# Performance work log

Measured on AMD Instinct MI355X. Metric: run time of the kernel, lower is better.

The kernel has to match this reference:

```python
import jax, jax.numpy as jnp
import numpy as np

CHANNELS = 512
NUM_HEADS = 8
GROUPS = 32
EPS = 1e-5


def setup_inputs() -> dict:
    key = jax.random.key(0)
    ks = jax.random.split(key, 7)
    C = CHANNELS
    x = jax.random.normal(ks[0], (8, C, 32, 32), dtype=jnp.float32)
    gn_weight = jnp.ones((C,), dtype=jnp.float32)
    gn_bias = jnp.zeros((C,), dtype=jnp.float32)
    # Conv1d(C, 3C, k=1) weights ~ N(0, 0.02) per init_weights
    qkv_w = 0.02 * jax.random.normal(ks[1], (3 * C, C), dtype=jnp.float32)
    qkv_b = 0.01 * jax.random.normal(ks[2], (3 * C,), dtype=jnp.float32)
    out_w = 0.02 * jax.random.normal(ks[3], (C, C), dtype=jnp.float32)
    out_b = 0.01 * jax.random.normal(ks[4], (C,), dtype=jnp.float32)
    return {"x": x, "gn_weight": gn_weight, "gn_bias": gn_bias,
            "qkv_w": qkv_w, "qkv_b": qkv_b, "out_w": out_w, "out_b": out_b}


def _forward(x, gn_weight, gn_bias, qkv_w, qkv_b, out_w, out_b):
    n, c, h, w = x.shape
    hw = h * w
    heads = NUM_HEADS
    cph = c // heads
    xs = x.reshape(n, c, hw)  # [N, C, HW]
    # GroupNorm over (channels-in-group, spatial)
    xg = xs.reshape(n, GROUPS, c // GROUPS, hw)
    mean = jnp.mean(xg, axis=(2, 3), keepdims=True)
    var = jnp.var(xg, axis=(2, 3), keepdims=True)
    xn = ((xg - mean) * jax.lax.rsqrt(var + EPS)).reshape(n, c, hw)
    xn = xn * gn_weight[None, :, None] + gn_bias[None, :, None]
    # 1x1 Conv1d QKV projection
    qkv = jnp.einsum('oc,ncl->nol', qkv_w, xn) + qkv_b[None, :, None]  # [N, 3C, HW]
    q, k, v = jnp.split(qkv, 3, axis=1)  # each [N, C, HW]
    q = q.reshape(n * heads, cph, hw)
    k = k.reshape(n * heads, cph, hw)
    v = v.reshape(n * heads, cph, hw)
    scale = 1.0 / np.sqrt(cph).astype(np.float32)
    scores = jnp.einsum('bci,bcj->bij', q, k) * scale  # [NH, HW, HW]
    attn = jax.nn.softmax(scores, axis=-1)
    weighted = jnp.einsum('bij,bcj->bic', attn, v)  # [NH, HW, cph]
    # Faithful to torch: reshape(n, -1, h, w) on [n*heads, hw, cph] layout
    weighted = weighted.reshape(n, c, h, w)
    out = jnp.einsum('oc,nchw->nohw', out_w, weighted) + out_b[None, :, None, None]
    return out


def reference(x, gn_weight, gn_bias, qkv_w, qkv_b, out_w, out_b):
    return _forward(x, gn_weight, gn_bias, qkv_w, qkv_b, out_w, out_b)
```

## Files before the change

### kernel.cpp

```cpp
#include <hip/hip_runtime.h>
#include <math.h>

#define N_    8
#define C_    512
#define HW_   1024
#define G_    32
#define CPG_  16
#define OC3_  1536
#define LOG2E 1.44269504f

typedef _Float16 f16;
typedef f16 f16x8 __attribute__((ext_vector_type(8)));
typedef f16 f16x4 __attribute__((ext_vector_type(4)));
typedef float f32x4 __attribute__((ext_vector_type(4)));

#define GLOAD_LDS16(g, l)                                                          \
    __builtin_amdgcn_global_load_lds(                                              \
        (const __attribute__((address_space(1))) unsigned int*)(const void*)(g),   \
        (__attribute__((address_space(3))) unsigned int*)(void*)(l), 16, 0, 0)

#define WAIT_VM0() __builtin_amdgcn_s_waitcnt(0x0F70)

__global__ __launch_bounds__(256) void prep(const float* __restrict__ x,
                                            const float* __restrict__ gw,
                                            const float* __restrict__ gb,
                                            f16* __restrict__ XT,
                                            const float* __restrict__ qkv_w,
                                            const float* __restrict__ out_w,
                                            const float* __restrict__ qkv_b,
                                            f16* __restrict__ Wq,
                                            f16* __restrict__ Wo,
                                            float* __restrict__ qkv_bs) {
    __shared__ float red1[4], red2[4];
    __shared__ float sm, srstd;
    if (blockIdx.x >= 256) {
        const float QS = 0.125f * LOG2E;
        int idx = (blockIdx.x - 256) * 256 + threadIdx.x;
        if (idx < 786432) {
            float v = qkv_w[idx];
            if (idx < 262144) v *= QS;
            Wq[idx] = (f16)v;
        } else if (idx < 786432 + 262144) {
            Wo[idx - 786432] = (f16)out_w[idx - 786432];
        } else if (idx < 786432 + 262144 + 1536) {
            int i = idx - 786432 - 262144;
            float v = qkv_b[i];
            if (i < 512) v *= QS;
            qkv_bs[i] = v;
        }
        return;
    }
    int blk = blockIdx.x;
    int n = blk >> 5, g = blk & 31;
    size_t base = ((size_t)n * C_ + (size_t)g * CPG_) * HW_;
    const float4* xp4 = (const float4*)(x + base);
    float4 vals[16];
    float s1 = 0.f, s2 = 0.f;
#pragma unroll
    for (int r = 0; r < 16; r++) {
        float4 v = xp4[r * 256 + threadIdx.x];
        vals[r] = v;
        s1 += v.x + v.y + v.z + v.w;
        s2 += v.x * v.x + v.y * v.y + v.z * v.z + v.w * v.w;
    }
#pragma unroll
    for (int off = 32; off > 0; off >>= 1) {
        s1 += __shfl_down(s1, off, 64);
        s2 += __shfl_down(s2, off, 64);
    }
    int wave = threadIdx.x >> 6, lane = threadIdx.x & 63;
    if (lane == 0) { red1[wave] = s1; red2[wave] = s2; }
    __syncthreads();
    if (threadIdx.x == 0) {
        float t1 = red1[0] + red1[1] + red1[2] + red1[3];
        float t2 = red2[0] + red2[1] + red2[2] + red2[3];
        float mean = t1 * (1.f / 16384.f);
        float var  = t2 * (1.f / 16384.f) - mean * mean;
        sm = mean;
        srstd = rsqrtf(var + 1e-5f);
    }
    __syncthreads();
    float mean = sm, rstd = srstd;
    float av[16], bbv[16];
#pragma unroll
    for (int r = 0; r < 16; r++) {
        int c = g * CPG_ + r;
        av[r] = gw[c] * rstd;
        bbv[r] = gb[c] - mean * av[r];
    }
    f16x8 lo[4], hi[4];
#pragma unroll
    for (int r = 0; r < 16; r++) {
        float4 v = vals[r];
        float a = av[r], bb = bbv[r];
        f16 e0 = (f16)(v.x * a + bb), e1 = (f16)(v.y * a + bb);
        f16 e2 = (f16)(v.z * a + bb), e3 = (f16)(v.w * a + bb);
        if (r < 8) { lo[0][r] = e0; lo[1][r] = e1; lo[2][r] = e2; lo[3][r] = e3; }
        else { hi[0][r - 8] = e0; hi[1][r - 8] = e1; hi[2][r - 8] = e2; hi[3][r - 8] = e3; }
    }
    f16* xt = XT + (size_t)n * C_ * HW_ + ((size_t)g * HW_ + threadIdx.x * 4) * 16;
#pragma unroll
    for (int comp = 0; comp < 4; comp++) {
        *(f16x8*)&xt[comp * 16]     = lo[comp];
        *(f16x8*)&xt[comp * 16 + 8] = hi[comp];
    }
}

template <bool FINAL>
__global__ __launch_bounds__(256, 4) void gemm_f16(const f16* __restrict__ A,
                                                   const f16* __restrict__ B,
                                                   const float* __restrict__ bias,
                                                   void* __restrict__ Yq,
                                                   f16* __restrict__ Yv) {
    __shared__ __align__(16) unsigned char smem[34816];
    f16* As = (f16*)smem;
    f16* Bs = (f16*)(smem + 16384);
    int tid = threadIdx.x, lane = tid & 63, w = tid >> 6;
    int m = lane & 15, quad = lane >> 4;
    int ow0 = (w & 1) * 64, lw0 = (w >> 1) * 64;
    int flat = blockIdx.x;
    int n = flat & 7, rest = flat >> 3;
    int l0 = (rest & 7) * 128, o0 = (rest >> 3) * 128;
    const f16* Bn = B + (size_t)n * C_ * HW_;

    int rowT[4], sgT[4];
#pragma unroll
    for (int t = 0; t < 4; t++) {
        int q = (w * 4 + t) * 64 + lane;
        int row = q >> 3, seg = q & 7;
        rowT[t] = row;
        sgT[t] = seg ^ (row & 7);
    }

    f32x4 acc[4][4];
#pragma unroll
    for (int i = 0; i < 4; i++)
#pragma unroll
        for (int j = 0; j < 4; j++)
#pragma unroll
            for (int r = 0; r < 4; r++) acc[i][j][r] = 0.f;

    for (int c0 = 0; c0 < 512; c0 += 64) {
        __syncthreads();
#pragma unroll
        for (int t = 0; t < 4; t++) {
            GLOAD_LDS16(A + (size_t)(o0 + rowT[t]) * 512 + c0 + sgT[t] * 8,
                        As + (size_t)(w * 4 + t) * 512);
            size_t baddr;
            if (FINAL) {
                baddr = (size_t)(l0 + rowT[t]) * 512 + c0 + sgT[t] * 8;
            } else {
                int c = c0 + sgT[t] * 8;
                baddr = ((size_t)(c >> 4) * HW_ + (l0 + rowT[t])) * 16 + (c & 15);
            }
            GLOAD_LDS16(Bn + baddr, Bs + (size_t)(w * 4 + t) * 512);
        }
        WAIT_VM0();
        __syncthreads();
#pragma unroll
        for (int ks = 0; ks < 2; ks++) {
            f16x8 af[4], bf[4];
#pragma unroll
            for (int ib = 0; ib < 4; ib++) {
                int row = ow0 + ib * 16 + m;
                int seg = (ks * 4 + quad) ^ (row & 7);
                af[ib] = *(const f16x8*)&As[row * 64 + seg * 8];
            }
#pragma unroll
            for (int jb = 0; jb < 4; jb++) {
                int row = lw0 + jb * 16 + m;
                int seg = (ks * 4 + quad) ^ (row & 7);
                bf[jb] = *(const f16x8*)&Bs[row * 64 + seg * 8];
            }
#pragma unroll
            for (int ib = 0; ib < 4; ib++)
#pragma unroll
                for (int jb = 0; jb < 4; jb++)
                    acc[ib][jb] = __builtin_amdgcn_mfma_f32_16x16x32_f16(
                        af[ib], bf[jb], acc[ib][jb], 0, 0, 0);
        }
    }

    float bv[4][4];
#pragma unroll
    for (int ib = 0; ib < 4; ib++)
#pragma unroll
        for (int r = 0; r < 4; r++)
            bv[ib][r] = bias[o0 + ow0 + ib * 16 + quad * 4 + r];

    if (FINAL) {
        float* on = (float*)Yq + (size_t)n * C_ * HW_;
#pragma unroll
        for (int ib = 0; ib < 4; ib++)
#pragma unroll
            for (int jb = 0; jb < 4; jb++)
#pragma unroll
                for (int r = 0; r < 4; r++)
                    on[(size_t)(o0 + ow0 + ib * 16 + quad * 4 + r) * HW_ +
                       l0 + lw0 + jb * 16 + m] = acc[ib][jb][r] + bv[ib][r];
    } else if (o0 >= 1024) {
        f16* vn = Yv + (size_t)n * C_ * HW_;
#pragma unroll
        for (int ib = 0; ib < 4; ib++)
#pragma unroll
            for (int jb = 0; jb < 4; jb++)
#pragma unroll
                for (int r = 0; r < 4; r++)
                    vn[(size_t)(o0 - 1024 + ow0 + ib * 16 + quad * 4 + r) * HW_ +
                       l0 + lw0 + jb * 16 + m] = (f16)(acc[ib][jb][r] + bv[ib][r]);
    } else {
        __syncthreads();
        f16* T = (f16*)smem;
#pragma unroll
        for (int ib = 0; ib < 4; ib++)
#pragma unroll
            for (int jb = 0; jb < 4; jb++) {
                f16x4 h;
#pragma unroll
                for (int r = 0; r < 4; r++) h[r] = (f16)(acc[ib][jb][r] + bv[ib][r]);
                int l = lw0 + jb * 16 + m;
                int oo = ow0 + ib * 16 + quad * 4;
                *(f16x4*)&T[l * 136 + oo] = h;
            }
        __syncthreads();
        f16* qn = (f16*)Yq + (size_t)n * HW_ * 1024;
#pragma unroll
        for (int rep = 0; rep < 8; rep++) {
            int idx = rep * 256 + tid;
            int l = idx >> 4, seg = idx & 15;
            f16x8 v = *(const f16x8*)&T[l * 136 + seg * 8];
            *(f16x8*)&qn[(size_t)(l0 + l) * 1024 + o0 + seg * 8] = v;
        }
    }
}

__global__ __launch_bounds__(256, 4) void attn_f16(const f16* __restrict__ qkvT,
                                                   const f16* __restrict__ vbuf,
                                                   f16* __restrict__ w2T) {
    __shared__ __align__(16) unsigned char smem[32768];
    f16* Kb0  = (f16*)smem;
    f16* Vb0  = (f16*)(smem + 16384);
    f16* LDSo = (f16*)smem;

    int tid = threadIdx.x;
    int lane = tid & 63, wave = tid >> 6;
    int m = lane & 15, quad = lane >> 4;
    int flat = blockIdx.x;
    int xcd = flat & 7, slot = flat >> 3;
    int itile = slot >> 3, bh = (slot & 7) * 8 + xcd;
    int n = bh >> 3, head = bh & 7;
    int i0 = itile * 64;
    const f16* qb = qkvT + (size_t)n * HW_ * 1024 + head * 64;
    const f16* kb = qb + 512;
    const f16* vb = vbuf + (size_t)n * C_ * HW_ + (size_t)head * 64 * HW_;

    const f16* qr = qb + (size_t)(i0 + wave * 16 + m) * 1024;
    f16x8 aq0 = *(const f16x8*)&qr[quad * 8];
    f16x8 aq1 = *(const f16x8*)&qr[32 + quad * 8];

#pragma unroll
    for (int it = 0; it < 2; it++) {
        int chunk = it * 256 + tid;
        int row = chunk >> 3, seg = chunk & 7;
        int segg = seg ^ (row & 7);
        GLOAD_LDS16(kb + (size_t)row * 1024 + segg * 8,
                    Kb0 + ((size_t)it * 256 + wave * 64) * 8);
        GLOAD_LDS16(vb + (size_t)row * HW_ + segg * 8,
                    Vb0 + ((size_t)it * 256 + wave * 64) * 8);
    }

    f32x4 oacc[4];
#pragma unroll
    for (int cb = 0; cb < 4; cb++)
#pragma unroll
        for (int r = 0; r < 4; r++) oacc[cb][r] = 0.f;
    float lsum = 0.f;
    int m7 = m & 7;

    for (int jt = 0; jt < 16; jt++) {
        int p = jt & 1;
        const f16* Kp = Kb0 + p * 4096;
        const f16* Vp = Vb0 + p * 4096;
        WAIT_VM0();
        __syncthreads();
        if (jt < 15) {
            int j0n = (jt + 1) * 64;
            f16* Kn = Kb0 + (1 - p) * 4096;
            f16* Vn = Vb0 + (1 - p) * 4096;
#pragma unroll
            for (int it = 0; it < 2; it++) {
                int chunk = it * 256 + tid;
                int row = chunk >> 3, seg = chunk & 7;
                int segg = seg ^ (row & 7);
                GLOAD_LDS16(kb + (size_t)(j0n + row) * 1024 + segg * 8,
                            Kn + ((size_t)it * 256 + wave * 64) * 8);
                GLOAD_LDS16(vb + (size_t)row * HW_ + j0n + segg * 8,
                            Vn + ((size_t)it * 256 + wave * 64) * 8);
            }
        }

        f16x8 kf[8];
#pragma unroll
        for (int jb = 0; jb < 4; jb++) {
            int row = jb * 16 + m;
            kf[jb]     = *(const f16x8*)&Kp[row * 64 + ((quad ^ (row & 7)) * 8)];
            kf[4 + jb] = *(const f16x8*)&Kp[row * 64 + (((4 + quad) ^ (row & 7)) * 8)];
        }

        f32x4 sacc[4];
#pragma unroll
        for (int jb = 0; jb < 4; jb++)
#pragma unroll
            for (int r = 0; r < 4; r++) sacc[jb][r] = 0.f;
#pragma unroll
        for (int jb = 0; jb < 4; jb++)
            sacc[jb] = __builtin_amdgcn_mfma_f32_16x16x32_f16(kf[jb], aq0,
                                                              sacc[jb], 0, 0, 0);
#pragma unroll
        for (int jb = 0; jb < 4; jb++)
            sacc[jb] = __builtin_amdgcn_mfma_f32_16x16x32_f16(kf[4 + jb], aq1,
                                                              sacc[jb], 0, 0, 0);

        f16x4 pf[4];
#pragma unroll
        for (int jb = 0; jb < 4; jb++) {
            float p0 = exp2f(sacc[jb][0]), p1 = exp2f(sacc[jb][1]);
            float p2 = exp2f(sacc[jb][2]), p3 = exp2f(sacc[jb][3]);
            lsum += (p0 + p1) + (p2 + p3);
            pf[jb][0] = (f16)p0; pf[jb][1] = (f16)p1;
            pf[jb][2] = (f16)p2; pf[jb][3] = (f16)p3;
        }

#pragma unroll
        for (int jb = 0; jb < 4; jb++) {
            int segb = jb * 2 + (quad >> 1);
#pragma unroll
            for (int cb = 0; cb < 4; cb++) {
                f16x4 vf4 = *(const f16x4*)&Vp[(cb * 16 + m) * 64 +
                                               ((segb ^ m7) * 8) + (quad & 1) * 4];
                oacc[cb] = __builtin_amdgcn_mfma_f32_16x16x16f16(pf[jb], vf4,
                                                                 oacc[cb], 0, 0, 0);
            }
        }
    }

    float ls = lsum;
    ls += __shfl_xor(ls, 16, 64);
    ls += __shfl_xor(ls, 32, 64);
    float linv[4];
#pragma unroll
    for (int r = 0; r < 4; r++) linv[r] = 1.f / __shfl(ls, quad * 4 + r, 64);

    WAIT_VM0();
    __syncthreads();
#pragma unroll
    for (int cb = 0; cb < 4; cb++)
#pragma unroll
        for (int r = 0; r < 4; r++) {
            int sc = (quad * 4 + r) * 64 + cb * 16 + m;
            LDSo[sc * 4 + wave] = (f16)(oacc[cb][r] * linv[r]);
        }
    __syncthreads();
    f16* w2n = w2T + (size_t)n * HW_ * 512;
    int chbase = head * 64 + (i0 >> 4);
#pragma unroll
    for (int it = 0; it < 4; it++) {
        int sc = it * 256 + tid;
        *(f16x4*)&w2n[(size_t)sc * 512 + chbase] = *(const f16x4*)&LDSo[sc * 4];
    }
}

extern "C" void kernel_launch(void* const* d_in, const int* in_sizes, int n_in,
                              void* d_out, int out_size, void* d_ws, size_t ws_size,
                              hipStream_t stream) {
    (void)in_sizes; (void)n_in; (void)out_size; (void)ws_size;
    const float* x     = (const float*)d_in[0];
    const float* gw    = (const float*)d_in[1];
    const float* gb    = (const float*)d_in[2];
    const float* qkv_w = (const float*)d_in[3];
    const float* qkv_b = (const float*)d_in[4];
    const float* out_w = (const float*)d_in[5];
    const float* out_b = (const float*)d_in[6];
    float* out = (float*)d_out;
    char* ws = (char*)d_ws;

    const size_t MB = 1024 * 1024;
    f16*   qkvT   = (f16*)ws;
    f16*   XT     = (f16*)(ws + 16 * MB);
    f16*   vbuf   = (f16*)(ws + 24 * MB);
    f16*   w2T    = (f16*)(ws + 32 * MB);
    f16*   Wq     = (f16*)(ws + 40 * MB);
    f16*   Wo     = (f16*)(ws + 42 * MB);
    float* qkv_bs = (float*)(ws + 43 * MB);

    prep<<<dim3(256 + 4103), 256, 0, stream>>>(x, gw, gb, XT,
                                               qkv_w, out_w, qkv_b, Wq, Wo, qkv_bs);
    gemm_f16<false><<<dim3(768), 256, 0, stream>>>(Wq, XT, qkv_bs, (void*)qkvT, vbuf);
    attn_f16<<<dim3(1024), 256, 0, stream>>>(qkvT, vbuf, w2T);
    gemm_f16<true><<<dim3(256), 256, 0, stream>>>(Wo, w2T, out_b, (void*)out, nullptr);
}
```

Baseline: 151.2 us.

## Double-buffer GEMM K-loop and halve output-projection M tile

The GEMM kernel now stages K in chunks of 32 into two LDS buffers and issues the global→LDS loads for the next chunk before computing the current one, so memory latency overlaps with MFMA work. The LDS swizzle is adjusted for the narrower rows. The final output-projection GEMM uses a 64-row M tile and launches twice as many blocks to fill more CUs. The cost is one barrier per 32-wide K step instead of per 64, and smaller per-wave MFMA tiles in the final GEMM.

```diff
diff --git a/kernel.cpp b/kernel.cpp
--- a/kernel.cpp
+++ b/kernel.cpp
@@ -112,78 +112,86 @@
                                                    const float* __restrict__ bias,
                                                    void* __restrict__ Yq,
                                                    f16* __restrict__ Yv) {
-    __shared__ __align__(16) unsigned char smem[34816];
-    f16* As = (f16*)smem;
-    f16* Bs = (f16*)(smem + 16384);
+    constexpr int BM = FINAL ? 64 : 128;
+    constexpr int MI = BM / 32;
+    constexpr int AB = BM * 64;
+    __shared__ __align__(16) unsigned char smem[FINAL ? 24576 : 34816];
     int tid = threadIdx.x, lane = tid & 63, w = tid >> 6;
     int m = lane & 15, quad = lane >> 4;
-    int ow0 = (w & 1) * 64, lw0 = (w >> 1) * 64;
+    int ow0 = (w & 1) * (BM / 2), lw0 = (w >> 1) * 64;
     int flat = blockIdx.x;
     int n = flat & 7, rest = flat >> 3;
-    int l0 = (rest & 7) * 128, o0 = (rest >> 3) * 128;
+    int l0 = (rest & 7) * 128, o0 = (rest >> 3) * BM;
     const f16* Bn = B + (size_t)n * C_ * HW_;
 
-    int rowT[4], sgT[4];
-#pragma unroll
-    for (int t = 0; t < 4; t++) {
-        int q = (w * 4 + t) * 64 + lane;
-        int row = q >> 3, seg = q & 7;
-        rowT[t] = row;
-        sgT[t] = seg ^ (row & 7);
-    }
-
-    f32x4 acc[4][4];
-#pragma unroll
-    for (int i = 0; i < 4; i++)
+    f32x4 acc[MI][4];
+#pragma unroll
+    for (int i = 0; i < MI; i++)
 #pragma unroll
         for (int j = 0; j < 4; j++)
 #pragma unroll
             for (int r = 0; r < 4; r++) acc[i][j][r] = 0.f;
 
-    for (int c0 = 0; c0 < 512; c0 += 64) {
-        __syncthreads();
-#pragma unroll
-        for (int t = 0; t < 4; t++) {
-            GLOAD_LDS16(A + (size_t)(o0 + rowT[t]) * 512 + c0 + sgT[t] * 8,
-                        As + (size_t)(w * 4 + t) * 512);
-            size_t baddr;
-            if (FINAL) {
-                baddr = (size_t)(l0 + rowT[t]) * 512 + c0 + sgT[t] * 8;
-            } else {
-                int c = c0 + sgT[t] * 8;
-                baddr = ((size_t)(c >> 4) * HW_ + (l0 + rowT[t])) * 16 + (c & 15);
-            }
-            GLOAD_LDS16(Bn + baddr, Bs + (size_t)(w * 4 + t) * 512);
-        }
+#define STAGE_STEP(c0_, pb_)                                                       \
+    do {                                                                           \
+        _Pragma("unroll")                                                          \
+        for (int it = 0; it < BM / 64; it++) {                                     \
+            int q = it * 256 + tid;                                                \
+            int row = q >> 2, sg = (q & 3) ^ ((row >> 1) & 3);                     \
+            GLOAD_LDS16(A + (size_t)(o0 + row) * 512 + (c0_) + sg * 8,             \
+                        (f16*)(smem + (pb_) * AB) + (size_t)(it * 256 + w * 64) * 8); \
+        }                                                                          \
+        _Pragma("unroll")                                                          \
+        for (int it = 0; it < 2; it++) {                                           \
+            int q = it * 256 + tid;                                                \
+            int row = q >> 2, sg = (q & 3) ^ ((row >> 1) & 3);                     \
+            size_t baddr;                                                          \
+            if (FINAL) {                                                           \
+                baddr = (size_t)(l0 + row) * 512 + (c0_) + sg * 8;                 \
+            } else {                                                               \
+                int c = (c0_) + sg * 8;                                            \
+                baddr = ((size_t)(c >> 4) * HW_ + (l0 + row)) * 16 + (c & 15);     \
+            }                                                                      \
+            GLOAD_LDS16(Bn + baddr,                                                \
+                        (f16*)(smem + 2 * AB + (pb_) * 8192) +                     \
+                            (size_t)(it * 256 + w * 64) * 8);                      \
+        }                                                                          \
+    } while (0)
+
+    STAGE_STEP(0, 0);
+
+    for (int cs = 0; cs < 16; cs++) {
+        int p = cs & 1;
         WAIT_VM0();
         __syncthreads();
-#pragma unroll
-        for (int ks = 0; ks < 2; ks++) {
-            f16x8 af[4], bf[4];
-#pragma unroll
-            for (int ib = 0; ib < 4; ib++) {
-                int row = ow0 + ib * 16 + m;
-                int seg = (ks * 4 + quad) ^ (row & 7);
-                af[ib] = *(const f16x8*)&As[row * 64 + seg * 8];
-            }
-#pragma unroll
-            for (int jb = 0; jb < 4; jb++) {
-                int row = lw0 + jb * 16 + m;
-                int seg = (ks * 4 + quad) ^ (row & 7);
-                bf[jb] = *(const f16x8*)&Bs[row * 64 + seg * 8];
-            }
-#pragma unroll
-            for (int ib = 0; ib < 4; ib++)
-#pragma unroll
-                for (int jb = 0; jb < 4; jb++)
-                    acc[ib][jb] = __builtin_amdgcn_mfma_f32_16x16x32_f16(
-                        af[ib], bf[jb], acc[ib][jb], 0, 0, 0);
-        }
-    }
-
-    float bv[4][4];
-#pragma unroll
-    for (int ib = 0; ib < 4; ib++)
+        if (cs < 15) STAGE_STEP((cs + 1) * 32, 1 - p);
+        const f16* Asp = (const f16*)(smem + p * AB);
+        const f16* Bsp = (const f16*)(smem + 2 * AB + p * 8192);
+        f16x8 af[MI], bf[4];
+#pragma unroll
+        for (int ib = 0; ib < MI; ib++) {
+            int row = ow0 + ib * 16 + m;
+            int sg = quad ^ ((row >> 1) & 3);
+            af[ib] = *(const f16x8*)&Asp[row * 32 + sg * 8];
+        }
+#pragma unroll
+        for (int jb = 0; jb < 4; jb++) {
+            int row = lw0 + jb * 16 + m;
+            int sg = quad ^ ((row >> 1) & 3);
+            bf[jb] = *(const f16x8*)&Bsp[row * 32 + sg * 8];
+        }
+#pragma unroll
+        for (int ib = 0; ib < MI; ib++)
+#pragma unroll
+            for (int jb = 0; jb < 4; jb++)
+                acc[ib][jb] = __builtin_amdgcn_mfma_f32_16x16x32_f16(
+                    af[ib], bf[jb], acc[ib][jb], 0, 0, 0);
+    }
+#undef STAGE_STEP
+
+    float bv[MI][4];
+#pragma unroll
+    for (int ib = 0; ib < MI; ib++)
 #pragma unroll
         for (int r = 0; r < 4; r++)
             bv[ib][r] = bias[o0 + ow0 + ib * 16 + quad * 4 + r];
@@ -191,7 +199,7 @@
     if (FINAL) {
         float* on = (float*)Yq + (size_t)n * C_ * HW_;
 #pragma unroll
-        for (int ib = 0; ib < 4; ib++)
+        for (int ib = 0; ib < MI; ib++)
 #pragma unroll
             for (int jb = 0; jb < 4; jb++)
 #pragma unroll
@@ -201,7 +209,7 @@
     } else if (o0 >= 1024) {
         f16* vn = Yv + (size_t)n * C_ * HW_;
 #pragma unroll
-        for (int ib = 0; ib < 4; ib++)
+        for (int ib = 0; ib < MI; ib++)
 #pragma unroll
             for (int jb = 0; jb < 4; jb++)
 #pragma unroll
@@ -212,7 +220,7 @@
         __syncthreads();
         f16* T = (f16*)smem;
 #pragma unroll
-        for (int ib = 0; ib < 4; ib++)
+        for (int ib = 0; ib < MI; ib++)
 #pragma unroll
             for (int jb = 0; jb < 4; jb++) {
                 f16x4 h;
@@ -397,5 +405,5 @@
                                                qkv_w, out_w, qkv_b, Wq, Wo, qkv_bs);
     gemm_f16<false><<<dim3(768), 256, 0, stream>>>(Wq, XT, qkv_bs, (void*)qkvT, vbuf);
     attn_f16<<<dim3(1024), 256, 0, stream>>>(qkvT, vbuf, w2T);
-    gemm_f16<true><<<dim3(256), 256, 0, stream>>>(Wo, w2T, out_b, (void*)out, nullptr);
+    gemm_f16<true><<<dim3(512), 256, 0, stream>>>(Wo, w2T, out_b, (void*)out, nullptr);
 }
```

Result: no change. 153.4 us (+1.4%).
